# Kernel optimization log

Hardware: AMD Instinct MI355X
Metric: run time of the kernel (lower is better)

## Reference

```python
import jax, jax.numpy as jnp
import numpy as np

EPS = 2.220446049250313e-16  # sys.float_info.epsilon
H_BW = 0.1  # bandwidth h


def setup_inputs() -> dict:
    key = jax.random.key(0)
    k1, k2 = jax.random.split(key)
    X = jax.random.normal(k1, (4, 256, 64, 64), dtype=jnp.float32)
    Y = jax.random.normal(k2, (4, 256, 64, 64), dtype=jnp.float32)
    return {"X_features": X, "Y_features": Y}


def _l2_normalize_c(f):
    # torch.norm(f, 2, dim=1, keepdim=True) + eps over channel dim of NCHW
    n = jnp.sqrt(jnp.sum(f * f, axis=1, keepdims=True)) + EPS
    return f / n


def reference(X_features, Y_features):
    B, C = X_features.shape[0], X_features.shape[1]
    # PONO centering: mean over channel dim of Y
    y_mean = jnp.mean(Y_features, axis=1, keepdims=True)  # [B,1,H,W]
    X = X_features - y_mean
    Y = Y_features - y_mean
    Xn = _l2_normalize_c(X).reshape(B, C, -1)  # [B,C,M]
    Yn = _l2_normalize_c(Y).reshape(B, C, -1)  # [B,C,M]
    # cosine distance matrix [B,M,M]
    d = 1.0 - jnp.einsum('bci,bcj->bij', Xn, Yn)
    d_norm = d / (jnp.min(d, axis=-1, keepdims=True) + 0.001)
    w = jnp.exp((1.0 - d_norm) / H_BW)
    A_ij = w / jnp.sum(w, axis=-1, keepdims=True)
    CX = jnp.mean(jnp.max(A_ij, axis=-1), axis=1)  # [B]
    return jnp.mean(-jnp.log(CX))
```

## Files before the change

### kernel.cpp

```cpp
#include <hip/hip_runtime.h>
#include <hip/hip_bf16.h>

typedef unsigned short u16;
typedef unsigned int u32;
typedef __attribute__((ext_vector_type(8))) __bf16 bf16x8;
typedef __attribute__((ext_vector_type(4))) float f32x4;
typedef __attribute__((ext_vector_type(8))) short short8;

#define EPSF 2.220446049250313e-16f

__device__ __forceinline__ u16 f2bf(float f) {
    u32 u = __float_as_uint(f);
    return (u16)((u + 0x7FFFu + ((u >> 16) & 1u)) >> 16);
}

__device__ __forceinline__ void gll16(const void* g, void* l) {
    __builtin_amdgcn_global_load_lds(
        (const __attribute__((address_space(1))) unsigned int*)g,
        (__attribute__((address_space(3))) unsigned int*)l, 16, 0, 0);
}

#define MEMFENCE asm volatile("" ::: "memory")
#define BAR() do { MEMFENCE; __builtin_amdgcn_s_barrier(); MEMFENCE; } while (0)
#define VMWAIT(N) do { asm volatile("s_waitcnt vmcnt(" #N ")" ::: "memory"); \
                       __builtin_amdgcn_sched_barrier(0); } while (0)

__global__ __launch_bounds__(256) void prep_kernel(
    const float* __restrict__ X, const float* __restrict__ Y,
    u16* __restrict__ XnT, u16* __restrict__ YnT)
{
    const int b  = blockIdx.x >> 6;
    const int p0 = (blockIdx.x & 63) << 6;
    const int t  = threadIdx.x;
    const int w  = t >> 6, l = t & 63;
    const size_t base = (size_t)b * 256 * 4096 + p0;

    __shared__ float T[64 * 261];
    __shared__ float pS[4][64], pSS[4][64];
    __shared__ float meanL[64], rnL[64];

    const int ch = t & 31, pxs = t >> 5;

    {
        float s1 = 0.f, s2 = 0.f;
        #pragma unroll 8
        for (int rep = 0; rep < 64; ++rep) {
            int c = rep * 4 + w;
            float v = Y[base + (size_t)c * 4096 + l];
            T[l * 261 + c] = v;
            s1 += v; s2 += v * v;
        }
        pS[w][l] = s1; pSS[w][l] = s2;
        __syncthreads();
        if (t < 64) {
            float Sy  = pS[0][t] + pS[1][t] + pS[2][t] + pS[3][t];
            float Syy = pSS[0][t] + pSS[1][t] + pSS[2][t] + pSS[3][t];
            float m = Sy * (1.f / 256.f);
            float ss = fmaxf(Syy - m * Sy, 0.f);
            meanL[t] = m;
            rnL[t] = 1.f / (sqrtf(ss) + EPSF);
        }
        __syncthreads();
        #pragma unroll
        for (int rep = 0; rep < 8; ++rep) {
            int px = rep * 8 + pxs;
            float m = meanL[px], rn = rnL[px];
            short8 h;
            #pragma unroll
            for (int k = 0; k < 8; ++k)
                h[k] = (short)f2bf((T[px * 261 + ch * 8 + k] - m) * rn);
            *(short8*)(YnT + ((size_t)b * 4096 + p0 + px) * 256 + ch * 8) = h;
        }
        __syncthreads();
    }
    {
        float s1 = 0.f, s2 = 0.f;
        #pragma unroll 8
        for (int rep = 0; rep < 64; ++rep) {
            int c = rep * 4 + w;
            float v = X[base + (size_t)c * 4096 + l];
            T[l * 261 + c] = v;
            s1 += v; s2 += v * v;
        }
        pS[w][l] = s1; pSS[w][l] = s2;
        __syncthreads();
        if (t < 64) {
            float Sx  = pS[0][t] + pS[1][t] + pS[2][t] + pS[3][t];
            float Sxx = pSS[0][t] + pSS[1][t] + pSS[2][t] + pSS[3][t];
            float m = meanL[t];
            float ss = fmaxf(Sxx - 2.f * m * Sx + 256.f * m * m, 0.f);
            rnL[t] = 1.f / (sqrtf(ss) + EPSF);
        }
        __syncthreads();
        #pragma unroll
        for (int rep = 0; rep < 8; ++rep) {
            int px = rep * 8 + pxs;
            float m = meanL[px], rn = rnL[px];
            short8 h;
            #pragma unroll
            for (int k = 0; k < 8; ++k)
                h[k] = (short)f2bf((T[px * 261 + ch * 8 + k] - m) * rn);
            *(short8*)(XnT + ((size_t)b * 4096 + p0 + px) * 256 + ch * 8) = h;
        }
    }
}

template <int PASS>
__global__ __launch_bounds__(256, 4) void cx_pass(
    const u16* __restrict__ XnT, const u16* __restrict__ YnT,
    const float* __restrict__ partIn, float* __restrict__ partOut)
{
    __shared__ u16 B0[16384];
    __shared__ u16 B1[16384];
    __shared__ float smxL[64];
    __shared__ float redL[64][2];

    const int t = threadIdx.x;
    const int w = t >> 6, l = t & 63;
    const int l15 = l & 15, g = l >> 4;
    const int wr = w >> 1, wc = w & 1;

    const int id = blockIdx.x;
    const int xcd = id & 7, slot = id >> 3;
    const int b = xcd >> 1;
    const int sub = ((xcd & 1) << 7) | slot;
    const int it = sub >> 2, jr = sub & 3;
    const int i0 = it << 6;
    const int j0 = jr << 10;

    const u16* Ab = XnT + ((size_t)b * 4096 + i0) * 256;
    const u16* Bb = YnT + ((size_t)b * 4096 + j0) * 256;

    bf16x8 a[2][8];
    #pragma unroll
    for (int fm = 0; fm < 2; ++fm)
        #pragma unroll
        for (int ks = 0; ks < 8; ++ks)
            a[fm][ks] = *(const bf16x8*)((const char*)Ab +
                (wr * 32 + fm * 16 + l15) * 512 + ks * 64 + g * 16);

    if (PASS == 1) {
        if (t < 64) {
            float4 v = *(const float4*)(partIn + ((size_t)b * 4096 + i0 + t) * 4);
            smxL[t] = fmaxf(fmaxf(v.x, v.y), fmaxf(v.z, v.w));
        }
        __syncthreads();
    }
    float itau[2][4], moff[2][4];
    if (PASS == 1) {
        #pragma unroll
        for (int fm = 0; fm < 2; ++fm)
            #pragma unroll
            for (int r = 0; r < 4; ++r) {
                float m = smxL[wr * 32 + fm * 16 + g * 4 + r];
                float iv = 14.4269504089f / (1.001f - m);
                itau[fm][r] = iv;
                moff[fm][r] = m * iv;
            }
    }

    float racc[2][4];
    #pragma unroll
    for (int fm = 0; fm < 2; ++fm)
        #pragma unroll
        for (int r = 0; r < 4; ++r) racc[fm][r] = (PASS == 0) ? -2.0f : 0.0f;

    const int srow0 = t >> 5;
    const int gch = (t & 31) ^ srow0;
    auto stage = [&](u16* dst, const u16* src) {
        #pragma unroll
        for (int q = 0; q < 8; ++q)
            gll16(src + (q * 8 + srow0) * 256 + gch * 8, dst + q * 2048 + w * 512);
    };

    const int swz = (l15 & 7) << 4;
    auto compute = [&](const u16* buf) {
        f32x4 acc[2][2] = {};
        #pragma unroll
        for (int ks = 0; ks < 8; ++ks) {
            const int kb = ks * 64 + g * 16;
            bf16x8 bf0 = *(const bf16x8*)((const char*)buf + (wc * 32 + l15) * 512 + (kb ^ swz));
            bf16x8 bf1 = *(const bf16x8*)((const char*)buf + (wc * 32 + 16 + l15) * 512 + (kb ^ swz));
            __builtin_amdgcn_s_setprio(1);
            acc[0][0] = __builtin_amdgcn_mfma_f32_16x16x32_bf16(a[0][ks], bf0, acc[0][0], 0, 0, 0);
            acc[0][1] = __builtin_amdgcn_mfma_f32_16x16x32_bf16(a[0][ks], bf1, acc[0][1], 0, 0, 0);
            acc[1][0] = __builtin_amdgcn_mfma_f32_16x16x32_bf16(a[1][ks], bf0, acc[1][0], 0, 0, 0);
            acc[1][1] = __builtin_amdgcn_mfma_f32_16x16x32_bf16(a[1][ks], bf1, acc[1][1], 0, 0, 0);
            __builtin_amdgcn_s_setprio(0);
        }
        #pragma unroll
        for (int fm = 0; fm < 2; ++fm)
            #pragma unroll
            for (int r = 0; r < 4; ++r) {
                if (PASS == 0) {
                    racc[fm][r] = fmaxf(racc[fm][r], fmaxf(acc[fm][0][r], acc[fm][1][r]));
                } else {
                    racc[fm][r] += exp2f(fmaf(acc[fm][0][r], itau[fm][r], -moff[fm][r]))
                                 + exp2f(fmaf(acc[fm][1][r], itau[fm][r], -moff[fm][r]));
                }
            }
    };

    const u16* src = Bb;
    stage(B0, src); src += 16384;
    #pragma unroll 1
    for (int s2 = 0; s2 < 8; ++s2) {
        stage(B1, src); src += 16384;
        VMWAIT(8); BAR();
        compute(B0);
        BAR();
        if (s2 < 7) {
            stage(B0, src); src += 16384;
            VMWAIT(8); BAR();
        } else {
            VMWAIT(0); BAR();
        }
        compute(B1);
        BAR();
    }

    #pragma unroll
    for (int fm = 0; fm < 2; ++fm)
        #pragma unroll
        for (int r = 0; r < 4; ++r) {
            float v = racc[fm][r];
            if (PASS == 0) {
                v = fmaxf(v, __shfl_xor(v, 1, 64));
                v = fmaxf(v, __shfl_xor(v, 2, 64));
                v = fmaxf(v, __shfl_xor(v, 4, 64));
                v = fmaxf(v, __shfl_xor(v, 8, 64));
            } else {
                v += __shfl_xor(v, 1, 64);
                v += __shfl_xor(v, 2, 64);
                v += __shfl_xor(v, 4, 64);
                v += __shfl_xor(v, 8, 64);
            }
            if (l15 == 0) redL[wr * 32 + fm * 16 + g * 4 + r][wc] = v;
        }
    __syncthreads();
    if (t < 64) {
        float res = (PASS == 0) ? fmaxf(redL[t][0], redL[t][1])
                                : redL[t][0] + redL[t][1];
        partOut[((size_t)b * 4096 + i0 + t) * 4 + jr] = res;
    }
}

__global__ __launch_bounds__(256) void csum_kernel(
    const float* __restrict__ p1, float* __restrict__ csum)
{
    __shared__ float rr[4];
    const int t = threadIdx.x;
    const int row = blockIdx.x * 256 + t;
    float4 v = *(const float4*)(p1 + (size_t)row * 4);
    float cx = 1.0f / ((v.x + v.y) + (v.z + v.w));
    #pragma unroll
    for (int sh = 1; sh <= 32; sh <<= 1) cx += __shfl_xor(cx, sh, 64);
    if ((t & 63) == 0) rr[t >> 6] = cx;
    __syncthreads();
    if (t == 0) csum[blockIdx.x] = rr[0] + rr[1] + rr[2] + rr[3];
}

__global__ __launch_bounds__(64) void final_kernel(
    const float* __restrict__ csum, float* __restrict__ out)
{
    __shared__ float rb[4];
    const int t = threadIdx.x;
    float v = csum[t];
    v += __shfl_xor(v, 1, 64);
    v += __shfl_xor(v, 2, 64);
    v += __shfl_xor(v, 4, 64);
    v += __shfl_xor(v, 8, 64);
    if ((t & 15) == 0) rb[t >> 4] = v;
    __syncthreads();
    if (t == 0) {
        float loss = 0.f;
        #pragma unroll
        for (int bb = 0; bb < 4; ++bb)
            loss += -logf(rb[bb] * (1.f / 4096.f));
        out[0] = loss * 0.25f;
    }
}

extern "C" void kernel_launch(void* const* d_in, const int* in_sizes, int n_in,
                              void* d_out, int out_size, void* d_ws, size_t ws_size,
                              hipStream_t stream)
{
    const float* X = (const float*)d_in[0];
    const float* Y = (const float*)d_in[1];
    char* ws = (char*)d_ws;
    u16* XnT = (u16*)(ws);
    u16* YnT = (u16*)(ws + (8u << 20));
    float* part0 = (float*)(ws + (16u << 20));
    float* part1 = (float*)(ws + (16u << 20) + (256u << 10));
    float* csum  = (float*)(ws + (16u << 20) + (512u << 10));
    float* out = (float*)d_out;

    hipLaunchKernelGGL(prep_kernel, dim3(256), dim3(256), 0, stream,
                       X, Y, XnT, YnT);
    hipLaunchKernelGGL((cx_pass<0>), dim3(1024), dim3(256), 0, stream,
                       XnT, YnT, part0, part0);
    hipLaunchKernelGGL((cx_pass<1>), dim3(1024), dim3(256), 0, stream,
                       XnT, YnT, part0, part1);
    hipLaunchKernelGGL(csum_kernel, dim3(64), dim3(256), 0, stream,
                       part1, csum);
    hipLaunchKernelGGL(final_kernel, dim3(1), dim3(64), 0, stream,
                       csum, out);
}
```

Measured before the change: 174.3 us.

## Pre-pack operands in MFMA fragment layout and drop LDS staging in cx passes

The prep kernel now writes normalized X and Y in a packed per-16-row MFMA fragment layout, so each lane can load bf16x8 operands directly from global memory with coalesced reads. The cx passes no longer use the LDS double-buffered global_load_lds pipeline or barriers. Each block covers 64 rows against half the columns, with each wave taking its own column slices and holding 4 A fragments in registers. Partial results are now split into 2 parts per row instead of 4. The aim is to cut LDS traffic and synchronisation, at the cost of relying on L2/global latency hiding with lower occupancy (launch bounds 2) and more registers.

Result: faster. 169.5 us (-2.8%).

```diff
diff --git a/kernel.cpp b/kernel.cpp
--- a/kernel.cpp
+++ b/kernel.cpp
@@ -14,213 +14,181 @@
     return (u16)((u + 0x7FFFu + ((u >> 16) & 1u)) >> 16);
 }
 
-__device__ __forceinline__ void gll16(const void* g, void* l) {
-    __builtin_amdgcn_global_load_lds(
-        (const __attribute__((address_space(1))) unsigned int*)g,
-        (__attribute__((address_space(3))) unsigned int*)l, 16, 0, 0);
-}
-
-#define MEMFENCE asm volatile("" ::: "memory")
-#define BAR() do { MEMFENCE; __builtin_amdgcn_s_barrier(); MEMFENCE; } while (0)
-#define VMWAIT(N) do { asm volatile("s_waitcnt vmcnt(" #N ")" ::: "memory"); \
-                       __builtin_amdgcn_sched_barrier(0); } while (0)
-
 __global__ __launch_bounds__(256) void prep_kernel(
     const float* __restrict__ X, const float* __restrict__ Y,
-    u16* __restrict__ XnT, u16* __restrict__ YnT)
-{
-    const int b  = blockIdx.x >> 6;
-    const int p0 = (blockIdx.x & 63) << 6;
-    const int t  = threadIdx.x;
-    const int w  = t >> 6, l = t & 63;
-    const size_t base = (size_t)b * 256 * 4096 + p0;
-
-    __shared__ float T[64 * 261];
-    __shared__ float pS[4][64], pSS[4][64];
-    __shared__ float meanL[64], rnL[64];
-
-    const int ch = t & 31, pxs = t >> 5;
+    u16* __restrict__ Xp, u16* __restrict__ Yp)
+{
+    const int blk = blockIdx.x;
+    const int b = blk >> 8;
+    const int fbase = blk & 255;
+    const int t = threadIdx.x;
+    const int px = t & 15, cg = t >> 4;
+    const int l = t & 63, wv = t >> 6;
+    const size_t base = (size_t)b * 256 * 4096 + (fbase << 4) + px;
+
+    __shared__ float pA[4][16], pB[4][16];
+    __shared__ float meanL[16], rnL[16];
+
+    const int ks = cg >> 1;
+    const int g0 = (cg & 1) << 1;
+    const size_t pbase = (size_t)b << 20;
+    const size_t addr0 = pbase + ((size_t)(fbase * 8 + ks) * 64 + g0 * 16 + px) * 8;
+
+    float vals[16];
 
     {
         float s1 = 0.f, s2 = 0.f;
-        #pragma unroll 8
-        for (int rep = 0; rep < 64; ++rep) {
-            int c = rep * 4 + w;
-            float v = Y[base + (size_t)c * 4096 + l];
-            T[l * 261 + c] = v;
-            s1 += v; s2 += v * v;
-        }
-        pS[w][l] = s1; pSS[w][l] = s2;
-        __syncthreads();
-        if (t < 64) {
-            float Sy  = pS[0][t] + pS[1][t] + pS[2][t] + pS[3][t];
-            float Syy = pSS[0][t] + pSS[1][t] + pSS[2][t] + pSS[3][t];
+        #pragma unroll
+        for (int k = 0; k < 16; ++k) {
+            float v = Y[base + (size_t)(cg * 16 + k) * 4096];
+            vals[k] = v; s1 += v; s2 += v * v;
+        }
+        s1 += __shfl_xor(s1, 16, 64); s2 += __shfl_xor(s2, 16, 64);
+        s1 += __shfl_xor(s1, 32, 64); s2 += __shfl_xor(s2, 32, 64);
+        if (l < 16) { pA[wv][l] = s1; pB[wv][l] = s2; }
+        __syncthreads();
+        if (t < 16) {
+            float Sy = pA[0][t] + pA[1][t] + pA[2][t] + pA[3][t];
+            float Syy = pB[0][t] + pB[1][t] + pB[2][t] + pB[3][t];
             float m = Sy * (1.f / 256.f);
-            float ss = fmaxf(Syy - m * Sy, 0.f);
             meanL[t] = m;
-            rnL[t] = 1.f / (sqrtf(ss) + EPSF);
-        }
-        __syncthreads();
-        #pragma unroll
-        for (int rep = 0; rep < 8; ++rep) {
-            int px = rep * 8 + pxs;
-            float m = meanL[px], rn = rnL[px];
-            short8 h;
-            #pragma unroll
-            for (int k = 0; k < 8; ++k)
-                h[k] = (short)f2bf((T[px * 261 + ch * 8 + k] - m) * rn);
-            *(short8*)(YnT + ((size_t)b * 4096 + p0 + px) * 256 + ch * 8) = h;
-        }
+            rnL[t] = 1.f / (sqrtf(fmaxf(Syy - m * Sy, 0.f)) + EPSF);
+        }
+        __syncthreads();
+        float m = meanL[px], rn = rnL[px];
+        short8 h0, h1;
+        #pragma unroll
+        for (int k = 0; k < 8; ++k) {
+            h0[k] = (short)f2bf((vals[k] - m) * rn);
+            h1[k] = (short)f2bf((vals[8 + k] - m) * rn);
+        }
+        *(short8*)(Yp + addr0) = h0;
+        *(short8*)(Yp + addr0 + 128) = h1;
         __syncthreads();
     }
     {
         float s1 = 0.f, s2 = 0.f;
-        #pragma unroll 8
-        for (int rep = 0; rep < 64; ++rep) {
-            int c = rep * 4 + w;
-            float v = X[base + (size_t)c * 4096 + l];
-            T[l * 261 + c] = v;
-            s1 += v; s2 += v * v;
-        }
-        pS[w][l] = s1; pSS[w][l] = s2;
-        __syncthreads();
-        if (t < 64) {
-            float Sx  = pS[0][t] + pS[1][t] + pS[2][t] + pS[3][t];
-            float Sxx = pSS[0][t] + pSS[1][t] + pSS[2][t] + pSS[3][t];
+        #pragma unroll
+        for (int k = 0; k < 16; ++k) {
+            float v = X[base + (size_t)(cg * 16 + k) * 4096];
+            vals[k] = v; s1 += v; s2 += v * v;
+        }
+        s1 += __shfl_xor(s1, 16, 64); s2 += __shfl_xor(s2, 16, 64);
+        s1 += __shfl_xor(s1, 32, 64); s2 += __shfl_xor(s2, 32, 64);
+        if (l < 16) { pA[wv][l] = s1; pB[wv][l] = s2; }
+        __syncthreads();
+        if (t < 16) {
+            float Sx = pA[0][t] + pA[1][t] + pA[2][t] + pA[3][t];
+            float Sxx = pB[0][t] + pB[1][t] + pB[2][t] + pB[3][t];
             float m = meanL[t];
-            float ss = fmaxf(Sxx - 2.f * m * Sx + 256.f * m * m, 0.f);
-            rnL[t] = 1.f / (sqrtf(ss) + EPSF);
-        }
-        __syncthreads();
-        #pragma unroll
-        for (int rep = 0; rep < 8; ++rep) {
-            int px = rep * 8 + pxs;
-            float m = meanL[px], rn = rnL[px];
-            short8 h;
-            #pragma unroll
-            for (int k = 0; k < 8; ++k)
-                h[k] = (short)f2bf((T[px * 261 + ch * 8 + k] - m) * rn);
-            *(short8*)(XnT + ((size_t)b * 4096 + p0 + px) * 256 + ch * 8) = h;
-        }
+            rnL[t] = 1.f / (sqrtf(fmaxf(Sxx - 2.f * m * Sx + 256.f * m * m, 0.f)) + EPSF);
+        }
+        __syncthreads();
+        float m = meanL[px], rn = rnL[px];
+        short8 h0, h1;
+        #pragma unroll
+        for (int k = 0; k < 8; ++k) {
+            h0[k] = (short)f2bf((vals[k] - m) * rn);
+            h1[k] = (short)f2bf((vals[8 + k] - m) * rn);
+        }
+        *(short8*)(Xp + addr0) = h0;
+        *(short8*)(Xp + addr0 + 128) = h1;
     }
 }
 
 template <int PASS>
-__global__ __launch_bounds__(256, 4) void cx_pass(
-    const u16* __restrict__ XnT, const u16* __restrict__ YnT,
+__global__ __launch_bounds__(256, 2) void cx_pass(
+    const u16* __restrict__ Xp, const u16* __restrict__ Yp,
     const float* __restrict__ partIn, float* __restrict__ partOut)
 {
-    __shared__ u16 B0[16384];
-    __shared__ u16 B1[16384];
     __shared__ float smxL[64];
-    __shared__ float redL[64][2];
+    __shared__ float redL[64][4];
 
     const int t = threadIdx.x;
     const int w = t >> 6, l = t & 63;
     const int l15 = l & 15, g = l >> 4;
-    const int wr = w >> 1, wc = w & 1;
+    const int wc = w;
 
     const int id = blockIdx.x;
     const int xcd = id & 7, slot = id >> 3;
     const int b = xcd >> 1;
-    const int sub = ((xcd & 1) << 7) | slot;
-    const int it = sub >> 2, jr = sub & 3;
-    const int i0 = it << 6;
-    const int j0 = jr << 10;
-
-    const u16* Ab = XnT + ((size_t)b * 4096 + i0) * 256;
-    const u16* Bb = YnT + ((size_t)b * 4096 + j0) * 256;
-
-    bf16x8 a[2][8];
-    #pragma unroll
-    for (int fm = 0; fm < 2; ++fm)
-        #pragma unroll
-        for (int ks = 0; ks < 8; ++ks)
-            a[fm][ks] = *(const bf16x8*)((const char*)Ab +
-                (wr * 32 + fm * 16 + l15) * 512 + ks * 64 + g * 16);
+    const int it2 = ((xcd & 1) << 5) | (slot >> 1);
+    const int jh = slot & 1;
+    const int i0 = it2 << 6;
+
+    const size_t pb = (size_t)b << 20;
 
     if (PASS == 1) {
         if (t < 64) {
-            float4 v = *(const float4*)(partIn + ((size_t)b * 4096 + i0 + t) * 4);
-            smxL[t] = fmaxf(fmaxf(v.x, v.y), fmaxf(v.z, v.w));
-        }
-        __syncthreads();
-    }
-    float itau[2][4], moff[2][4];
+            float2 v = ((const float2*)partIn)[(size_t)b * 4096 + i0 + t];
+            smxL[t] = fmaxf(v.x, v.y);
+        }
+        __syncthreads();
+    }
+
+    bf16x8 a[4][8];
+    {
+        const u16* Apl = Xp + pb + (size_t)l * 8;
+        #pragma unroll
+        for (int fm = 0; fm < 4; ++fm)
+            #pragma unroll
+            for (int ks = 0; ks < 8; ++ks)
+                a[fm][ks] = *(const bf16x8*)(Apl + (size_t)(((i0 >> 4) + fm) * 8 + ks) * 512);
+    }
+
+    float mo[4][4], it_[4][4];
     if (PASS == 1) {
         #pragma unroll
-        for (int fm = 0; fm < 2; ++fm)
+        for (int fm = 0; fm < 4; ++fm)
             #pragma unroll
             for (int r = 0; r < 4; ++r) {
-                float m = smxL[wr * 32 + fm * 16 + g * 4 + r];
+                float m = smxL[fm * 16 + g * 4 + r];
                 float iv = 14.4269504089f / (1.001f - m);
-                itau[fm][r] = iv;
-                moff[fm][r] = m * iv;
-            }
-    }
-
-    float racc[2][4];
+                it_[fm][r] = iv;
+                mo[fm][r] = m * iv;
+            }
+    }
+
+    float racc[4][4];
     #pragma unroll
-    for (int fm = 0; fm < 2; ++fm)
+    for (int fm = 0; fm < 4; ++fm)
         #pragma unroll
         for (int r = 0; r < 4; ++r) racc[fm][r] = (PASS == 0) ? -2.0f : 0.0f;
 
-    const int srow0 = t >> 5;
-    const int gch = (t & 31) ^ srow0;
-    auto stage = [&](u16* dst, const u16* src) {
-        #pragma unroll
-        for (int q = 0; q < 8; ++q)
-            gll16(src + (q * 8 + srow0) * 256 + gch * 8, dst + q * 2048 + w * 512);
-    };
-
-    const int swz = (l15 & 7) << 4;
-    auto compute = [&](const u16* buf) {
-        f32x4 acc[2][2] = {};
+    const u16* Bpl = Yp + pb + (size_t)l * 8 + (size_t)(jh * 128 + wc) * 4096;
+    #pragma unroll 1
+    for (int u = 0; u < 32; ++u) {
+        const u16* bp = Bpl + (size_t)u * 16384;
+        f32x4 acc0 = {}, acc1 = {}, acc2 = {}, acc3 = {};
         #pragma unroll
         for (int ks = 0; ks < 8; ++ks) {
-            const int kb = ks * 64 + g * 16;
-            bf16x8 bf0 = *(const bf16x8*)((const char*)buf + (wc * 32 + l15) * 512 + (kb ^ swz));
-            bf16x8 bf1 = *(const bf16x8*)((const char*)buf + (wc * 32 + 16 + l15) * 512 + (kb ^ swz));
-            __builtin_amdgcn_s_setprio(1);
-            acc[0][0] = __builtin_amdgcn_mfma_f32_16x16x32_bf16(a[0][ks], bf0, acc[0][0], 0, 0, 0);
-            acc[0][1] = __builtin_amdgcn_mfma_f32_16x16x32_bf16(a[0][ks], bf1, acc[0][1], 0, 0, 0);
-            acc[1][0] = __builtin_amdgcn_mfma_f32_16x16x32_bf16(a[1][ks], bf0, acc[1][0], 0, 0, 0);
-            acc[1][1] = __builtin_amdgcn_mfma_f32_16x16x32_bf16(a[1][ks], bf1, acc[1][1], 0, 0, 0);
-            __builtin_amdgcn_s_setprio(0);
-        }
-        #pragma unroll
-        for (int fm = 0; fm < 2; ++fm)
+            bf16x8 bv = *(const bf16x8*)(bp + (ks << 9));
+            acc0 = __builtin_amdgcn_mfma_f32_16x16x32_bf16(a[0][ks], bv, acc0, 0, 0, 0);
+            acc1 = __builtin_amdgcn_mfma_f32_16x16x32_bf16(a[1][ks], bv, acc1, 0, 0, 0);
+            acc2 = __builtin_amdgcn_mfma_f32_16x16x32_bf16(a[2][ks], bv, acc2, 0, 0, 0);
+            acc3 = __builtin_amdgcn_mfma_f32_16x16x32_bf16(a[3][ks], bv, acc3, 0, 0, 0);
+        }
+        if (PASS == 0) {
             #pragma unroll
             for (int r = 0; r < 4; ++r) {
-                if (PASS == 0) {
-                    racc[fm][r] = fmaxf(racc[fm][r], fmaxf(acc[fm][0][r], acc[fm][1][r]));
-                } else {
-                    racc[fm][r] += exp2f(fmaf(acc[fm][0][r], itau[fm][r], -moff[fm][r]))
-                                 + exp2f(fmaf(acc[fm][1][r], itau[fm][r], -moff[fm][r]));
-                }
-            }
-    };
-
-    const u16* src = Bb;
-    stage(B0, src); src += 16384;
-    #pragma unroll 1
-    for (int s2 = 0; s2 < 8; ++s2) {
-        stage(B1, src); src += 16384;
-        VMWAIT(8); BAR();
-        compute(B0);
-        BAR();
-        if (s2 < 7) {
-            stage(B0, src); src += 16384;
-            VMWAIT(8); BAR();
+                racc[0][r] = fmaxf(racc[0][r], acc0[r]);
+                racc[1][r] = fmaxf(racc[1][r], acc1[r]);
+                racc[2][r] = fmaxf(racc[2][r], acc2[r]);
+                racc[3][r] = fmaxf(racc[3][r], acc3[r]);
+            }
         } else {
-            VMWAIT(0); BAR();
-        }
-        compute(B1);
-        BAR();
+            #pragma unroll
+            for (int r = 0; r < 4; ++r) {
+                racc[0][r] += exp2f(__builtin_fmaf(acc0[r], it_[0][r], -mo[0][r]));
+                racc[1][r] += exp2f(__builtin_fmaf(acc1[r], it_[1][r], -mo[1][r]));
+                racc[2][r] += exp2f(__builtin_fmaf(acc2[r], it_[2][r], -mo[2][r]));
+                racc[3][r] += exp2f(__builtin_fmaf(acc3[r], it_[3][r], -mo[3][r]));
+            }
+        }
     }
 
     #pragma unroll
-    for (int fm = 0; fm < 2; ++fm)
+    for (int fm = 0; fm < 4; ++fm)
         #pragma unroll
         for (int r = 0; r < 4; ++r) {
             float v = racc[fm][r];
@@ -235,13 +203,15 @@
                 v += __shfl_xor(v, 4, 64);
                 v += __shfl_xor(v, 8, 64);
             }
-            if (l15 == 0) redL[wr * 32 + fm * 16 + g * 4 + r][wc] = v;
+            if (l15 == 0) redL[fm * 16 + g * 4 + r][wc] = v;
         }
     __syncthreads();
     if (t < 64) {
-        float res = (PASS == 0) ? fmaxf(redL[t][0], redL[t][1])
-                                : redL[t][0] + redL[t][1];
-        partOut[((size_t)b * 4096 + i0 + t) * 4 + jr] = res;
+        float4 vv = *(const float4*)&redL[t][0];
+        float res = (PASS == 0)
+            ? fmaxf(fmaxf(vv.x, vv.y), fmaxf(vv.z, vv.w))
+            : (vv.x + vv.y) + (vv.z + vv.w);
+        partOut[((size_t)b * 4096 + i0 + t) * 2 + jh] = res;
     }
 }
 
@@ -251,8 +221,8 @@
     __shared__ float rr[4];
     const int t = threadIdx.x;
     const int row = blockIdx.x * 256 + t;
-    float4 v = *(const float4*)(p1 + (size_t)row * 4);
-    float cx = 1.0f / ((v.x + v.y) + (v.z + v.w));
+    float2 v = ((const float2*)p1)[row];
+    float cx = 1.0f / (v.x + v.y);
     #pragma unroll
     for (int sh = 1; sh <= 32; sh <<= 1) cx += __shfl_xor(cx, sh, 64);
     if ((t & 63) == 0) rr[t >> 6] = cx;
@@ -288,19 +258,19 @@
     const float* X = (const float*)d_in[0];
     const float* Y = (const float*)d_in[1];
     char* ws = (char*)d_ws;
-    u16* XnT = (u16*)(ws);
-    u16* YnT = (u16*)(ws + (8u << 20));
+    u16* Xp = (u16*)(ws);
+    u16* Yp = (u16*)(ws + (8u << 20));
     float* part0 = (float*)(ws + (16u << 20));
-    float* part1 = (float*)(ws + (16u << 20) + (256u << 10));
-    float* csum  = (float*)(ws + (16u << 20) + (512u << 10));
+    float* part1 = (float*)(ws + (16u << 20) + (128u << 10));
+    float* csum  = (float*)(ws + (16u << 20) + (256u << 10));
     float* out = (float*)d_out;
 
-    hipLaunchKernelGGL(prep_kernel, dim3(256), dim3(256), 0, stream,
-                       X, Y, XnT, YnT);
-    hipLaunchKernelGGL((cx_pass<0>), dim3(1024), dim3(256), 0, stream,
-                       XnT, YnT, part0, part0);
-    hipLaunchKernelGGL((cx_pass<1>), dim3(1024), dim3(256), 0, stream,
-                       XnT, YnT, part0, part1);
+    hipLaunchKernelGGL(prep_kernel, dim3(1024), dim3(256), 0, stream,
+                       X, Y, Xp, Yp);
+    hipLaunchKernelGGL((cx_pass<0>), dim3(512), dim3(256), 0, stream,
+                       Xp, Yp, part0, part0);
+    hipLaunchKernelGGL((cx_pass<1>), dim3(512), dim3(256), 0, stream,
+                       Xp, Yp, part0, part1);
     hipLaunchKernelGGL(csum_kernel, dim3(64), dim3(256), 0, stream,
                        part1, csum);
     hipLaunchKernelGGL(final_kernel, dim3(1), dim3(64), 0, stream,
```
